# Optimization experiments

Hardware: AMD Instinct MI355X
Metric: run time of the kernel (lower is better)

The kernel has to match this reference:

```python
import jax, jax.numpy as jnp
import numpy as np

# Model dims (see init_kwargs)
NU = 4096   # num_users (one-hot feature dim)
NV = 4096   # num_items
C = 5       # num_classes (rating levels)
H0 = 256    # hidden[0]
H1 = 128    # hidden[1]
D_IN = 512  # input_dim (side-feature dense dim)
SIDE = 1024 # raw side-feature dim (u_features.size(1))
NB = 2      # nb basis matrices in bilinear decoder


def setup_inputs() -> dict:
    key = jax.random.key(0)
    ks = jax.random.split(key, 16)
    u = jax.random.randint(ks[0], (4096,), 0, NU)
    v = jax.random.randint(ks[1], (4096,), 0, NV)
    r = jax.random.randint(ks[2], (4096,), 0, C)  # unused by forward (as in source)
    raw = jax.random.randint(ks[3], (NU, NV), 0, 4 * C)
    adj_matrix = (raw[None, :, :] == jnp.arange(1, C + 1)[:, None, None]).astype(jnp.float32)
    u_features = jax.random.normal(ks[4], (NU, SIDE), jnp.float32)
    v_features = jax.random.normal(ks[5], (NV, SIDE), jnp.float32)
    def w(k, shape, fan):
        return jax.random.normal(k, shape, jnp.float32) / np.float32(np.sqrt(fan))
    u_w = w(ks[6], (C, NU, H0), NU)          # per-relation GraphConvolution user weights
    v_w = w(ks[7], (C, NV, H0), NV)          # per-relation item weights
    Wu1 = w(ks[8], (D_IN, SIDE), SIDE); bu1 = jnp.zeros((D_IN,), jnp.float32)
    Wv1 = w(ks[9], (D_IN, SIDE), SIDE); bv1 = jnp.zeros((D_IN,), jnp.float32)
    Wu2 = w(ks[10], (H1, D_IN + H0), D_IN + H0)
    Wv2 = w(ks[11], (H1, D_IN + H0), D_IN + H0)
    P = w(ks[12], (NB, H1, H1), H1)          # bilinear basis matrices
    a = w(ks[13], (NB, C), NB)               # basis -> class coefficients
    return dict(u=u, v=v, r=r, adj_matrix=adj_matrix, u_features=u_features,
                v_features=v_features, u_w=u_w, v_w=v_w, Wu1=Wu1, bu1=bu1,
                Wv1=Wv1, bv1=bv1, Wu2=Wu2, Wv2=Wv2, P=P, a=a)


def reference(u, v, r, adj_matrix, u_features, v_features, u_w, v_w,
              Wu1, bu1, Wv1, bv1, Wu2, Wv2, P, a):
    # m = adj[:, u][:, :, v]  -> [C, nu, nv]
    m = adj_matrix[:, u][:, :, v]
    # degree normalization exactly as written in gc_encoder
    du = jnp.abs(m.sum(axis=1).sum(axis=0))   # [nv]
    di = jnp.abs(m.sum(axis=2).sum(axis=0))   # [nu]
    c = 1.0 / jnp.concatenate([du, di], axis=0)
    c = jnp.where(jnp.isinf(c), jnp.zeros_like(c), c)
    # ordinal weight sharing: W_r = sum_{s<=r} Theta_s; one-hot feat @ W == gather rows
    cu = jnp.cumsum(u_w, axis=0)              # [C, NU, H0]
    cv = jnp.cumsum(v_w, axis=0)
    u_x = cu[:, u]                            # [C, nu, H0]
    v_x = cv[:, v]                            # [C, nv, H0]
    # accumulate per-relation message passing across all C relations at once
    u_next = jnp.einsum('ruv,rvh->uh', m, v_x)   # [nu, H0]
    v_next = jnp.einsum('ruv,ruh->vh', m, u_x)   # [nv, H0]
    z = jax.nn.relu(jnp.concatenate([u_next, v_next], axis=0) * c[:, None])
    nu = u.shape[0]
    u_z, v_z = z[:nu], z[nu:]
    u_f = jax.nn.relu(u_features[u] @ Wu1.T + bu1)
    v_f = jax.nn.relu(v_features[v] @ Wv1.T + bv1)
    u_h = jax.nn.relu(jnp.concatenate([u_z, u_f], axis=1) @ Wu2.T)   # [nu, H1]
    v_h = jax.nn.relu(jnp.concatenate([v_z, v_f], axis=1) @ Wv2.T)   # [nv, H1]
    # bilinear mixture decoder: logits[c,u,v] = sum_b a[b,c] * u_h Q_b v_h^T
    outputs = jnp.einsum('ud,bde,ve,bc->cuv', u_h, P, v_h, a)        # [C, nu, nv]
    logp = jax.nn.log_softmax(outputs, axis=0)
    prob = jnp.exp(logp)
    ratings = jnp.arange(1, C + 1, dtype=outputs.dtype)
    m_hat = jnp.einsum('c,cuv->uv', ratings, prob)
    # losses over observed entries
    mask = m.sum(axis=0) > 0
    n_obs = jnp.maximum(mask.sum(), 1).astype(outputs.dtype)
    loss = -(m * logp).sum() / n_obs
    target = (jnp.argmax(m, axis=0) + 1).astype(outputs.dtype)
    se = jnp.where(mask, (m_hat - target) ** 2, jnp.zeros_like(m_hat))
    rmse_loss = jnp.sqrt(se.sum() / n_obs)
    return (m_hat, loss, rmse_loss)
```

## Files before the change

kernel.cpp:

```cpp
#include <hip/hip_runtime.h>
#include <stdint.h>

#define N4   4096
#define H0   256
#define SIDE 1024
#define DIN  512
#define HCAT 768
#define H1   128
#define NC   5
#define NUV  16777216ULL
#define CAP  1536

typedef __attribute__((ext_vector_type(8))) short short8;
typedef __attribute__((ext_vector_type(4))) float floatx4;

__device__ __forceinline__ unsigned short f2bf(float f) {
    unsigned int u;
    __builtin_memcpy(&u, &f, 4);
    unsigned int r = (u + 0x7FFFu + ((u >> 16) & 1u)) >> 16;
    return (unsigned short)r;
}

__device__ __forceinline__ float bf2f(unsigned short b) {
    unsigned int u = (unsigned int)b << 16;
    float f;
    __builtin_memcpy(&f, &u, 4);
    return f;
}

__global__ __launch_bounds__(256) void k_codeF(const float* __restrict__ adj,
                                               uchar4* __restrict__ code4,
                                               const int* __restrict__ u,
                                               const int* __restrict__ v,
                                               int* __restrict__ cu,
                                               int* __restrict__ cv) {
    int b = blockIdx.x, t = threadIdx.x;
    if (b < 16384) {
        size_t g = (size_t)b * 256 + t;
        size_t base = g * 4;
        uchar4 out = {0, 0, 0, 0};
        #pragma unroll
        for (int c = 0; c < NC; c++) {
            float4 s = *(const float4*)(adj + (size_t)c * NUV + base);
            out.x = (s.x != 0.f) ? (unsigned char)(c + 1) : out.x;
            out.y = (s.y != 0.f) ? (unsigned char)(c + 1) : out.y;
            out.z = (s.z != 0.f) ? (unsigned char)(c + 1) : out.z;
            out.w = (s.w != 0.f) ? (unsigned char)(c + 1) : out.w;
        }
        code4[g] = out;
    } else {
        int i = (b - 16384) * 256 + t;
        atomicAdd(&cu[u[i]], 1);
        atomicAdd(&cv[v[i]], 1);
    }
}

__global__ __launch_bounds__(256) void k_fuse0(const uint8_t* __restrict__ code,
                                               uint8_t* __restrict__ codeT,
                                               const float* __restrict__ u_w,
                                               const int* __restrict__ cnt_u,
                                               unsigned short* __restrict__ T_Au,
                                               const float* __restrict__ v_w,
                                               const int* __restrict__ cnt_v,
                                               unsigned short* __restrict__ T_Bv) {
    __shared__ __align__(16) uint8_t tile[64][80];
    int b = blockIdx.x, t = threadIdx.x;
    if (b < 4096) {
        int bx = b & 63, by = b >> 6;
        int row = t >> 2;
        int seg = (t & 3) * 16;
        int p0 = by * 64, q0 = bx * 64;
        uint4 vdat = *(const uint4*)(code + (size_t)(p0 + row) * N4 + q0 + seg);
        *(uint4*)(&tile[row][seg]) = vdat;
        __syncthreads();
        union { uint4 u4; uint8_t bb[16]; } o;
        #pragma unroll
        for (int l = 0; l < 16; l++) o.bb[l] = tile[seg + l][row];
        *(uint4*)(codeT + (size_t)(q0 + row) * N4 + p0 + seg) = o.u4;
    } else {
        int node = (b - 4096) & 4095;
        int side = (b - 4096) >> 12;
        const float* w = side ? v_w : u_w;
        const int* cnt = side ? cnt_v : cnt_u;
        unsigned short* out = side ? T_Bv : T_Au;
        int h = t;
        float c = (float)cnt[node];
        float acc = 0.f;
        #pragma unroll
        for (int r = 0; r < NC; r++) {
            size_t idx = ((size_t)r * N4 + node) * H0 + h;
            acc += w[idx];
            union { _Float16 h16; unsigned short s; } cvt;
            cvt.h16 = (_Float16)(acc * c);
            out[idx] = cvt.s;
        }
    }
}

__global__ __launch_bounds__(256) void k_compactF(const uint8_t* __restrict__ code,
                                                  const uint8_t* __restrict__ codeT,
                                                  const int* __restrict__ cnt_u,
                                                  const int* __restrict__ cnt_v,
                                                  unsigned short* __restrict__ idxU,
                                                  int* __restrict__ nnzU,
                                                  float* __restrict__ rowDeg,
                                                  unsigned short* __restrict__ idxV,
                                                  int* __restrict__ nnzV,
                                                  float* __restrict__ colDeg) {
    __shared__ float cw[4096];
    __shared__ int wtot[4];
    __shared__ float wdeg[4];
    __shared__ unsigned short ebuf[CAP];
    int side = blockIdx.y;
    const uint8_t* codeRows = side ? codeT : code;
    const int* cntOther = side ? cnt_u : cnt_v;
    unsigned short* idx = side ? idxV : idxU;
    int* nnz = side ? nnzV : nnzU;
    float* deg = side ? colDeg : rowDeg;

    int p = blockIdx.x, t = threadIdx.x;
    int lane = t & 63, wv = t >> 6;
    const int4* co4 = (const int4*)cntOther;
    #pragma unroll
    for (int l = 0; l < 4; l++) {
        int4 ci = co4[t + l * 256];
        ((float4*)cw)[t + l * 256] =
            make_float4((float)ci.x, (float)ci.y, (float)ci.z, (float)ci.w);
    }
    uint4 w = ((const uint4*)(codeRows + (size_t)p * N4))[t];
    unsigned char b[16];
    __builtin_memcpy(b, &w, 16);
    int cnt = 0;
    #pragma unroll
    for (int j = 0; j < 16; j++) cnt += (b[j] != 0);
    int sc = cnt;
    #pragma unroll
    for (int off = 1; off < 64; off <<= 1) {
        int up = __shfl_up(sc, off, 64);
        if (lane >= off) sc += up;
    }
    if (lane == 63) wtot[wv] = sc;
    __syncthreads();
    int wbase = 0;
    #pragma unroll
    for (int ww = 0; ww < 4; ww++) wbase += (ww < wv) ? wtot[ww] : 0;
    int total = wtot[0] + wtot[1] + wtot[2] + wtot[3];
    int pos = wbase + sc - cnt;
    float dsum = 0.f;
    #pragma unroll
    for (int j = 0; j < 16; j++) {
        int r = b[j];
        if (r) {
            int q = t * 16 + j;
            if (pos < CAP) ebuf[pos] = (unsigned short)((r - 1) * N4 + q);
            pos++;
            dsum += cw[q];
        }
    }
    #pragma unroll
    for (int off = 32; off; off >>= 1) dsum += __shfl_down(dsum, off, 64);
    if (lane == 0) wdeg[wv] = dsum;
    __syncthreads();
    int tw = total < CAP ? total : CAP;
    if (t == 0) { deg[p] = wdeg[0] + wdeg[1] + wdeg[2] + wdeg[3]; nnz[p] = tw; }
    for (int e = t; e < tw; e += 256) idx[(size_t)p * CAP + e] = ebuf[e];
}

__global__ __launch_bounds__(256) void k_gatherF(const unsigned short* __restrict__ idxU,
                                                 const int* __restrict__ nnzU,
                                                 const unsigned short* __restrict__ T_Bv,
                                                 float* __restrict__ u_nn,
                                                 const unsigned short* __restrict__ idxV,
                                                 const int* __restrict__ nnzV,
                                                 const unsigned short* __restrict__ T_Au,
                                                 float* __restrict__ v_nn) {
    __shared__ unsigned short sidx[CAP];
    __shared__ float red[16][132];
    int side = blockIdx.z;
    const unsigned short* idx = side ? idxV : idxU;
    const int* nnz = side ? nnzV : nnzU;
    const char* tb = (const char*)(side ? T_Au : T_Bv);
    float* outNN = side ? v_nn : u_nn;

    int p = blockIdx.x, half = blockIdx.y, t = threadIdx.x;
    int n = nnz[p];
    const unsigned short* rowIdx = idx + (size_t)p * CAP;
    for (int i = t; i < n; i += 256) sidx[i] = rowIdx[i];
    __syncthreads();
    int s = t >> 4;
    int c = t & 15;
    int boff = half * 256 + c * 16;
    float acc[8] = {0.f, 0.f, 0.f, 0.f, 0.f, 0.f, 0.f, 0.f};
    int nmain = n & ~63;
    for (int e = s; e < nmain; e += 64) {
        int o0 = ((int)sidx[e])      << 9;
        int o1 = ((int)sidx[e + 16]) << 9;
        int o2 = ((int)sidx[e + 32]) << 9;
        int o3 = ((int)sidx[e + 48]) << 9;
        uint4 d0 = *(const uint4*)(tb + o0 + boff);
        uint4 d1 = *(const uint4*)(tb + o1 + boff);
        uint4 d2 = *(const uint4*)(tb + o2 + boff);
        uint4 d3 = *(const uint4*)(tb + o3 + boff);
        union { uint4 u; _Float16 h[8]; } cv;
        cv.u = d0;
        #pragma unroll
        for (int k = 0; k < 8; k++) acc[k] += (float)cv.h[k];
        cv.u = d1;
        #pragma unroll
        for (int k = 0; k < 8; k++) acc[k] += (float)cv.h[k];
        cv.u = d2;
        #pragma unroll
        for (int k = 0; k < 8; k++) acc[k] += (float)cv.h[k];
        cv.u = d3;
        #pragma unroll
        for (int k = 0; k < 8; k++) acc[k] += (float)cv.h[k];
    }
    for (int e = nmain + s; e < n; e += 16) {
        int o = ((int)sidx[e]) << 9;
        uint4 d = *(const uint4*)(tb + o + boff);
        union { uint4 u; _Float16 h[8]; } cv;
        cv.u = d;
        #pragma unroll
        for (int k = 0; k < 8; k++) acc[k] += (float)cv.h[k];
    }
    #pragma unroll
    for (int k = 0; k < 8; k++) red[s][c * 8 + k] = acc[k];
    __syncthreads();
    if (t < 128) {
        float sum = 0.f;
        #pragma unroll
        for (int ss = 0; ss < 16; ss++) sum += red[ss][t];
        outNN[(size_t)p * H0 + half * 128 + t] = sum;
    }
}

__global__ __launch_bounds__(256) void k_fuse1(const uint8_t* __restrict__ code,
                                               const int* __restrict__ u,
                                               const int* __restrict__ v,
                                               uint8_t* __restrict__ codeR,
                                               const float* __restrict__ u_nn,
                                               const float* __restrict__ v_nn,
                                               const float* __restrict__ colDeg,
                                               const float* __restrict__ rowDeg,
                                               unsigned short* __restrict__ chiU,
                                               unsigned short* __restrict__ cloU,
                                               unsigned short* __restrict__ chiV,
                                               unsigned short* __restrict__ cloV,
                                               const float* __restrict__ u_feat,
                                               unsigned short* __restrict__ fuhi,
                                               unsigned short* __restrict__ fulo,
                                               const float* __restrict__ v_feat,
                                               unsigned short* __restrict__ fvhi,
                                               unsigned short* __restrict__ fvlo,
                                               const float* __restrict__ Wu1,
                                               unsigned short* __restrict__ wuhi,
                                               unsigned short* __restrict__ wulo,
                                               const float* __restrict__ Wv1,
                                               unsigned short* __restrict__ wvhi,
                                               unsigned short* __restrict__ wvlo,
                                               const float* __restrict__ Wu2,
                                               unsigned short* __restrict__ w2uhi,
                                               unsigned short* __restrict__ w2ulo,
                                               const float* __restrict__ Wv2,
                                               unsigned short* __restrict__ w2vhi,
                                               unsigned short* __restrict__ w2vlo,
                                               const float* __restrict__ P,
                                               float* __restrict__ Pt) {
    __shared__ __align__(16) uint8_t rowbuf[4096];
    int b = blockIdx.x, t = threadIdx.x;
    if (b < 4096) {
        int i = b;
        int urow = u[i];
        ((uint4*)rowbuf)[t] = ((const uint4*)(code + (size_t)urow * N4))[t];
        __syncthreads();
        uint8_t ob[16];
        #pragma unroll
        for (int w = 0; w < 4; w++) {
            int4 vv = ((const int4*)v)[t * 4 + w];
            ob[w * 4 + 0] = rowbuf[vv.x];
            ob[w * 4 + 1] = rowbuf[vv.y];
            ob[w * 4 + 2] = rowbuf[vv.z];
            ob[w * 4 + 3] = rowbuf[vv.w];
        }
        uint4 o;
        __builtin_memcpy(&o, ob, 16);
        ((uint4*)(codeR + (size_t)i * N4))[t] = o;
        return;
    }
    if (b < 12288) {
        int i = (b - 4096) & 4095;
        int side = (b - 4096) >> 12;
        const float* nn = side ? v_nn : u_nn;
        const int* idxs = side ? v : u;
        const int* idxo = side ? u : v;
        const float* deg = side ? rowDeg : colDeg;
        unsigned short* catHi = side ? chiV : chiU;
        unsigned short* catLo = side ? cloV : cloU;
        int h = t;
        float d = deg[idxo[i]];
        float inv = d > 0.f ? 1.f / d : 0.f;
        float val = fmaxf(nn[(size_t)idxs[i] * H0 + h] * inv, 0.f);
        unsigned short hb = f2bf(val);
        catHi[(size_t)i * HCAT + h] = hb;
        catLo[(size_t)i * HCAT + h] = f2bf(val - bf2f(hb));
        return;
    }
    if (b >= 21696) {
        int tid = (b - 21696) * 256 + t;
        int bb = tid >> 14;
        int d = (tid >> 7) & 127;
        int e = tid & 127;
        Pt[((size_t)bb * 128 + e) * 128 + d] = P[tid];
        return;
    }
    const float* src;
    unsigned short* hi;
    unsigned short* lo;
    int lb;
    if (b < 16384)      { src = u_feat; hi = fuhi; lo = fulo; lb = b - 12288; }
    else if (b < 20480) { src = v_feat; hi = fvhi; lo = fvlo; lb = b - 16384; }
    else if (b < 20992) { src = Wu1; hi = wuhi; lo = wulo; lb = b - 20480; }
    else if (b < 21504) { src = Wv1; hi = wvhi; lo = wvlo; lb = b - 20992; }
    else if (b < 21600) { src = Wu2; hi = w2uhi; lo = w2ulo; lb = b - 21504; }
    else                { src = Wv2; hi = w2vhi; lo = w2vlo; lb = b - 21600; }
    size_t g = ((size_t)lb * 256 + t) * 4;
    float4 x = *(const float4*)(src + g);
    float f[4] = {x.x, x.y, x.z, x.w};
    unsigned short hh[4], ll[4];
    #pragma unroll
    for (int k = 0; k < 4; k++) {
        unsigned short hb = f2bf(f[k]);
        hh[k] = hb;
        ll[k] = f2bf(f[k] - bf2f(hb));
    }
    *(ushort4*)(hi + g) = make_ushort4(hh[0], hh[1], hh[2], hh[3]);
    *(ushort4*)(lo + g) = make_ushort4(ll[0], ll[1], ll[2], ll[3]);
}

__global__ __launch_bounds__(256) void k_l1F(const unsigned short* __restrict__ fuhi,
                                             const unsigned short* __restrict__ fulo,
                                             const unsigned short* __restrict__ fvhi,
                                             const unsigned short* __restrict__ fvlo,
                                             const int* __restrict__ u,
                                             const int* __restrict__ v,
                                             const unsigned short* __restrict__ wuhi,
                                             const unsigned short* __restrict__ wulo,
                                             const unsigned short* __restrict__ wvhi,
                                             const unsigned short* __restrict__ wvlo,
                                             const float* __restrict__ bu1,
                                             const float* __restrict__ bv1,
                                             unsigned short* __restrict__ chiU,
                                             unsigned short* __restrict__ cloU,
                                             unsigned short* __restrict__ chiV,
                                             unsigned short* __restrict__ cloV) {
    __shared__ unsigned short Bh[64][72];
    __shared__ unsigned short Bl[64][72];
    int side = blockIdx.z;
    const unsigned short* Ahi = side ? fvhi : fuhi;
    const unsigned short* Alo = side ? fvlo : fulo;
    const int* rowmap = side ? v : u;
    const unsigned short* Bhi = side ? wvhi : wuhi;
    const unsigned short* Blo = side ? wvlo : wulo;
    const float* bias = side ? bv1 : bu1;
    unsigned short* CHi = (side ? chiV : chiU) + H0;
    unsigned short* CLo = (side ? cloV : cloU) + H0;

    int t = threadIdx.x;
    int wave = t >> 6, lane = t & 63;
    int lr = lane & 15;
    int lk = lane >> 4;
    int i0 = blockIdx.y * 64 + wave * 16;
    int n0 = blockIdx.x * 64;
    int gi = rowmap[i0 + lr];
    const unsigned short* pah = Ahi + (size_t)gi * SIDE;
    const unsigned short* pal = Alo + (size_t)gi * SIDE;
    int srow = t >> 2, sseg = (t & 3) * 16;
    floatx4 acc[4];
    #pragma unroll
    for (int jt = 0; jt < 4; jt++) acc[jt] = (floatx4){0.f, 0.f, 0.f, 0.f};
    for (int ks = 0; ks < SIDE / 64; ks++) {
        const unsigned short* sh = Bhi + (size_t)(n0 + srow) * SIDE + ks * 64 + sseg;
        const unsigned short* sl = Blo + (size_t)(n0 + srow) * SIDE + ks * 64 + sseg;
        __syncthreads();
        *(uint4*)(&Bh[srow][sseg]) = *(const uint4*)sh;
        *(uint4*)(&Bh[srow][sseg + 8]) = *(const uint4*)(sh + 8);
        *(uint4*)(&Bl[srow][sseg]) = *(const uint4*)sl;
        *(uint4*)(&Bl[srow][sseg + 8]) = *(const uint4*)(sl + 8);
        __syncthreads();
        #pragma unroll
        for (int kk = 0; kk < 2; kk++) {
            int ko = ks * 64 + kk * 32 + lk * 8;
            short8 ah = *(const short8*)(pah + ko);
            short8 al = *(const short8*)(pal + ko);
            #pragma unroll
            for (int jt = 0; jt < 4; jt++) {
                short8 bh = *(const short8*)(&Bh[jt * 16 + lr][kk * 32 + lk * 8]);
                short8 bl = *(const short8*)(&Bl[jt * 16 + lr][kk * 32 + lk * 8]);
                acc[jt] = __builtin_amdgcn_mfma_f32_16x16x32_bf16(ah, bh, acc[jt], 0, 0, 0);
                acc[jt] = __builtin_amdgcn_mfma_f32_16x16x32_bf16(ah, bl, acc[jt], 0, 0, 0);
                acc[jt] = __builtin_amdgcn_mfma_f32_16x16x32_bf16(al, bh, acc[jt], 0, 0, 0);
            }
        }
    }
    #pragma unroll
    for (int jt = 0; jt < 4; jt++) {
        int cn = n0 + jt * 16 + lr;
        float bb = bias[cn];
        #pragma unroll
        for (int r = 0; r < 4; r++) {
            int ci = i0 + lk * 4 + r;
            float vv = fmaxf(acc[jt][r] + bb, 0.f);
            unsigned short hb = f2bf(vv);
            CHi[(size_t)ci * HCAT + cn] = hb;
            CLo[(size_t)ci * HCAT + cn] = f2bf(vv - bf2f(hb));
        }
    }
}

__global__ __launch_bounds__(256) void k_l2F(const unsigned short* __restrict__ chiU,
                                             const unsigned short* __restrict__ cloU,
                                             const unsigned short* __restrict__ w2uhi,
                                             const unsigned short* __restrict__ w2ulo,
                                             float* __restrict__ uh,
                                             const unsigned short* __restrict__ chiV,
                                             const unsigned short* __restrict__ cloV,
                                             const unsigned short* __restrict__ w2vhi,
                                             const unsigned short* __restrict__ w2vlo,
                                             unsigned short* __restrict__ vhb) {
    __shared__ unsigned short Bh[64][72];
    __shared__ unsigned short Bl[64][72];
    int side = blockIdx.z;
    const unsigned short* Ahi = side ? chiV : chiU;
    const unsigned short* Alo = side ? cloV : cloU;
    const unsigned short* Bhi = side ? w2vhi : w2uhi;
    const unsigned short* Blo = side ? w2vlo : w2ulo;

    int t = threadIdx.x;
    int wave = t >> 6, lane = t & 63;
    int lr = lane & 15;
    int lk = lane >> 4;
    int i0 = blockIdx.y * 64 + wave * 16;
    int n0 = blockIdx.x * 64;
    const unsigned short* pah = Ahi + (size_t)(i0 + lr) * HCAT;
    const unsigned short* pal = Alo + (size_t)(i0 + lr) * HCAT;
    int srow = t >> 2, sseg = (t & 3) * 16;
    floatx4 acc[4];
    #pragma unroll
    for (int jt = 0; jt < 4; jt++) acc[jt] = (floatx4){0.f, 0.f, 0.f, 0.f};
    for (int ks = 0; ks < HCAT / 64; ks++) {
        const unsigned short* sh = Bhi + (size_t)(n0 + srow) * HCAT + ks * 64 + sseg;
        const unsigned short* sl = Blo + (size_t)(n0 + srow) * HCAT + ks * 64 + sseg;
        __syncthreads();
        *(uint4*)(&Bh[srow][sseg]) = *(const uint4*)sh;
        *(uint4*)(&Bh[srow][sseg + 8]) = *(const uint4*)(sh + 8);
        *(uint4*)(&Bl[srow][sseg]) = *(const uint4*)sl;
        *(uint4*)(&Bl[srow][sseg + 8]) = *(const uint4*)(sl + 8);
        __syncthreads();
        #pragma unroll
        for (int kk = 0; kk < 2; kk++) {
            int ko = ks * 64 + kk * 32 + lk * 8;
            short8 ah = *(const short8*)(pah + ko);
            short8 al = *(const short8*)(pal + ko);
            #pragma unroll
            for (int jt = 0; jt < 4; jt++) {
                short8 bh = *(const short8*)(&Bh[jt * 16 + lr][kk * 32 + lk * 8]);
                short8 bl = *(const short8*)(&Bl[jt * 16 + lr][kk * 32 + lk * 8]);
                acc[jt] = __builtin_amdgcn_mfma_f32_16x16x32_bf16(ah, bh, acc[jt], 0, 0, 0);
                acc[jt] = __builtin_amdgcn_mfma_f32_16x16x32_bf16(ah, bl, acc[jt], 0, 0, 0);
                acc[jt] = __builtin_amdgcn_mfma_f32_16x16x32_bf16(al, bh, acc[jt], 0, 0, 0);
            }
        }
    }
    #pragma unroll
    for (int jt = 0; jt < 4; jt++) {
        int cn = n0 + jt * 16 + lr;
        #pragma unroll
        for (int r = 0; r < 4; r++) {
            int ci = i0 + lk * 4 + r;
            float vv = fmaxf(acc[jt][r], 0.f);
            if (side) {
                vhb[(size_t)ci * H1 + cn] = f2bf(vv);
            } else {
                uh[(size_t)ci * H1 + cn] = vv;
            }
        }
    }
}

template <int TM, int TN, int BK, int RM, int RN>
__global__ __launch_bounds__(256) void k_gemm(const float* __restrict__ A, int lda,
                                              const float* __restrict__ B, int ldb,
                                              float* __restrict__ C, int ldc, int K,
                                              size_t bzs, size_t czs) {
    constexpr int TX = TN / RN;
    constexpr int TY = TM / RM;
    static_assert(TX * TY == 256, "block must be 256");
    __shared__ float As[BK][TM + 4];
    __shared__ float Bs[BK][TN + 4];
    int tid = threadIdx.x;
    int tx = tid % TX, ty = tid / TX;
    int i0 = blockIdx.x * TM, n0 = blockIdx.y * TN;
    const float* Bz = B + (size_t)blockIdx.z * bzs;
    float acc[RM][RN] = {};
    for (int k0 = 0; k0 < K; k0 += BK) {
        for (int g = tid; g < TM * BK / 4; g += 256) {
            int i = g / (BK / 4), kc = g % (BK / 4);
            float4 val = *(const float4*)(A + (size_t)(i0 + i) * lda + k0 + kc * 4);
            As[kc * 4 + 0][i] = val.x; As[kc * 4 + 1][i] = val.y;
            As[kc * 4 + 2][i] = val.z; As[kc * 4 + 3][i] = val.w;
        }
        for (int g = tid; g < TN * BK / 4; g += 256) {
            int n = g / (BK / 4), kc = g % (BK / 4);
            float4 val = *(const float4*)(Bz + (size_t)(n0 + n) * ldb + k0 + kc * 4);
            Bs[kc * 4 + 0][n] = val.x; Bs[kc * 4 + 1][n] = val.y;
            Bs[kc * 4 + 2][n] = val.z; Bs[kc * 4 + 3][n] = val.w;
        }
        __syncthreads();
        #pragma unroll
        for (int k = 0; k < BK; k++) {
            float av[RM], bv[RN];
            #pragma unroll
            for (int m = 0; m < RM; m++) av[m] = As[k][ty * RM + m];
            #pragma unroll
            for (int n = 0; n < RN; n++) bv[n] = Bs[k][tx * RN + n];
            #pragma unroll
            for (int m = 0; m < RM; m++)
                #pragma unroll
                for (int n = 0; n < RN; n++)
                    acc[m][n] = fmaf(av[m], bv[n], acc[m][n]);
        }
        __syncthreads();
    }
    #pragma unroll
    for (int m = 0; m < RM; m++) {
        int ig = i0 + ty * RM + m;
        #pragma unroll
        for (int n = 0; n < RN; n++) {
            unsigned short* Cz16 = (unsigned short*)C + (size_t)blockIdx.z * czs;
            Cz16[(size_t)ig * ldc + n0 + tx * RN + n] = f2bf(acc[m][n]);
        }
    }
}

__global__ __launch_bounds__(256) void k_scores3(const unsigned short* __restrict__ tb,
                                                 const unsigned short* __restrict__ vhb,
                                                 const uint8_t* __restrict__ codeR,
                                                 const float* __restrict__ a_f,
                                                 float* __restrict__ mhat,
                                                 float* __restrict__ part) {
    __shared__ float wred[4][3];
    int t = threadIdx.x;
    int wave = t >> 6, lane = t & 63;
    int lr = lane & 15;
    int lk = lane >> 4;
    int i0 = blockIdx.y * 64 + wave * 16;
    int j0 = blockIdx.x * 128;
    float sa0[NC], sa1[NC];
    #pragma unroll
    for (int c = 0; c < NC; c++) { sa0[c] = a_f[c]; sa1[c] = a_f[5 + c]; }

    const unsigned short* t0p = tb;
    const unsigned short* t1p = tb + (size_t)N4 * H1;
    short8 a0[4], a1[4];
    #pragma unroll
    for (int kc = 0; kc < 4; kc++) {
        size_t off = (size_t)(i0 + lr) * H1 + kc * 32 + lk * 8;
        a0[kc] = *(const short8*)(t0p + off);
        a1[kc] = *(const short8*)(t1p + off);
    }

    const uint8_t* crbase = codeR + (size_t)(i0 + lk * 4) * N4 + lr;
    short8 bcur[4];
    int cbv[4];
    {
        int jb = j0;
        const uint8_t* crp = crbase + jb;
        cbv[0] = crp[0];
        cbv[1] = crp[N4];
        cbv[2] = crp[2 * N4];
        cbv[3] = crp[3 * N4];
        #pragma unroll
        for (int kc = 0; kc < 4; kc++)
            bcur[kc] = *(const short8*)(vhb + (size_t)(jb + lr) * H1 + kc * 32 + lk * 8);
    }

    float lsum = 0.f, ssum = 0.f, nobs = 0.f;
    for (int jt = 0; jt < 8; jt++) {
        int jb = j0 + jt * 16;
        int j = jb + lr;
        short8 bnext[4];
        int cbn[4];
        if (jt < 7) {
            int jb2 = jb + 16;
            const uint8_t* crp = crbase + jb2;
            cbn[0] = crp[0];
            cbn[1] = crp[N4];
            cbn[2] = crp[2 * N4];
            cbn[3] = crp[3 * N4];
            #pragma unroll
            for (int kc = 0; kc < 4; kc++)
                bnext[kc] = *(const short8*)(vhb + (size_t)(jb2 + lr) * H1 + kc * 32 + lk * 8);
        }
        floatx4 C0 = {0.f, 0.f, 0.f, 0.f}, C1 = {0.f, 0.f, 0.f, 0.f};
        #pragma unroll
        for (int kc = 0; kc < 4; kc++) {
            C0 = __builtin_amdgcn_mfma_f32_16x16x32_bf16(a0[kc], bcur[kc], C0, 0, 0, 0);
            C1 = __builtin_amdgcn_mfma_f32_16x16x32_bf16(a1[kc], bcur[kc], C1, 0, 0, 0);
        }
        #pragma unroll
        for (int r = 0; r < 4; r++) {
            int i = i0 + lk * 4 + r;
            float v0 = C0[r], v1 = C1[r];
            float l[NC];
            float mx = -1e30f;
            #pragma unroll
            for (int c = 0; c < NC; c++) {
                l[c] = sa0[c] * v0 + sa1[c] * v1;
                mx = fmaxf(mx, l[c]);
            }
            float den = 0.f, num = 0.f;
            #pragma unroll
            for (int c = 0; c < NC; c++) {
                float e = __expf(l[c] - mx);
                den += e;
                num += (float)(c + 1) * e;
            }
            float mh = num / den;
            mhat[(size_t)i * N4 + j] = mh;
            int cb = cbv[r];
            if (cb) {
                float lse = mx + __logf(den);
                lsum += lse - l[cb - 1];
                float df = mh - (float)cb;
                ssum += df * df;
                nobs += 1.f;
            }
        }
        if (jt < 7) {
            #pragma unroll
            for (int kc = 0; kc < 4; kc++) bcur[kc] = bnext[kc];
            #pragma unroll
            for (int r = 0; r < 4; r++) cbv[r] = cbn[r];
        }
    }
    #pragma unroll
    for (int off = 32; off; off >>= 1) {
        lsum += __shfl_down(lsum, off, 64);
        ssum += __shfl_down(ssum, off, 64);
        nobs += __shfl_down(nobs, off, 64);
    }
    if (lane == 0) { wred[wave][0] = lsum; wred[wave][1] = ssum; wred[wave][2] = nobs; }
    __syncthreads();
    if (t == 0) {
        int bid = blockIdx.y * gridDim.x + blockIdx.x;
        part[bid * 3 + 0] = wred[0][0] + wred[1][0] + wred[2][0] + wred[3][0];
        part[bid * 3 + 1] = wred[0][1] + wred[1][1] + wred[2][1] + wred[3][1];
        part[bid * 3 + 2] = wred[0][2] + wred[1][2] + wred[2][2] + wred[3][2];
    }
}

__global__ __launch_bounds__(256) void k_finalize(const float* __restrict__ part,
                                                  float* __restrict__ out) {
    __shared__ float sred[3][4];
    int t = threadIdx.x, lane = t & 63, wv = t >> 6;
    float l = 0.f, s = 0.f, n = 0.f;
    for (int i = t; i < 2048; i += 256) {
        l += part[i * 3 + 0];
        s += part[i * 3 + 1];
        n += part[i * 3 + 2];
    }
    #pragma unroll
    for (int off = 32; off; off >>= 1) {
        l += __shfl_down(l, off, 64);
        s += __shfl_down(s, off, 64);
        n += __shfl_down(n, off, 64);
    }
    if (lane == 0) { sred[0][wv] = l; sred[1][wv] = s; sred[2][wv] = n; }
    __syncthreads();
    if (t == 0) {
        float L = sred[0][0] + sred[0][1] + sred[0][2] + sred[0][3];
        float S = sred[1][0] + sred[1][1] + sred[1][2] + sred[1][3];
        float N = fmaxf(sred[2][0] + sred[2][1] + sred[2][2] + sred[2][3], 1.f);
        out[NUV + 0] = L / N;
        out[NUV + 1] = sqrtf(S / N);
    }
}

extern "C" void kernel_launch(void* const* d_in, const int* in_sizes, int n_in,
                              void* d_out, int out_size, void* d_ws, size_t ws_size,
                              hipStream_t stream) {
    const int* u = (const int*)d_in[0];
    const int* v = (const int*)d_in[1];
    const float* adj    = (const float*)d_in[3];
    const float* u_feat = (const float*)d_in[4];
    const float* v_feat = (const float*)d_in[5];
    const float* u_w    = (const float*)d_in[6];
    const float* v_w    = (const float*)d_in[7];
    const float* Wu1    = (const float*)d_in[8];
    const float* bu1    = (const float*)d_in[9];
    const float* Wv1    = (const float*)d_in[10];
    const float* bv1    = (const float*)d_in[11];
    const float* Wu2    = (const float*)d_in[12];
    const float* Wv2    = (const float*)d_in[13];
    const float* P      = (const float*)d_in[14];
    const float* a      = (const float*)d_in[15];
    float* out = (float*)d_out;

    char* ws = (char*)d_ws;
    const size_t O_CODE  = 0;
    const size_t O_CNTU  = 16777216;
    const size_t O_CNTV  = O_CNTU + 16384;
    const size_t O_ACC   = O_CNTV + 16384;
    const size_t O_TAU   = O_ACC + 256;
    const size_t O_TBV   = O_TAU + 10485760;
    const size_t O_IDXU  = O_TBV + 10485760;
    const size_t O_IDXV  = O_IDXU + 12582912;
    const size_t O_NNZU  = O_IDXV + 12582912;
    const size_t O_NNZV  = O_NNZU + 16384;
    const size_t O_RDEG  = O_NNZV + 16384;
    const size_t O_CDEG  = O_RDEG + 16384;
    const size_t O_UNN   = O_CDEG + 16384;
    const size_t O_VNN   = O_UNN + 4194304;
    const size_t O_UCAT  = O_VNN + 4194304;
    const size_t O_VCAT  = O_UCAT + 12582912;
    const size_t O_UH    = O_VCAT + 12582912;
    const size_t O_VHB   = O_UH + 2097152;
    const size_t O_PT    = O_VHB + 1048576;
    const size_t O_TB    = O_PT + 131072;
    const size_t O_CODET = O_UCAT;
    const size_t O_CODER = O_TAU;
    const size_t O_PART  = O_CNTU;
    const size_t O_FUHI  = O_IDXU;
    const size_t O_FULO  = O_IDXV;
    const size_t O_CHIU  = O_UCAT;
    const size_t O_CLOU  = O_UCAT + 6291456;
    const size_t O_CHIV  = O_VCAT;
    const size_t O_CLOV  = O_VCAT + 6291456;
    const size_t S_FVHI  = 0;
    const size_t S_FVLO  = 8388608;
    const size_t S_WUHI  = 16777216;
    const size_t S_WULO  = S_WUHI + 1048576;
    const size_t S_WVHI  = S_WULO + 1048576;
    const size_t S_WVLO  = S_WVHI + 1048576;
    const size_t S_W2UHI = S_WVLO + 1048576;
    const size_t S_W2ULO = S_W2UHI + 196608;
    const size_t S_W2VHI = S_W2ULO + 196608;
    const size_t S_W2VLO = S_W2VHI + 196608;

    uint8_t* code  = (uint8_t*)(ws + O_CODE);
    uint8_t* codeT = (uint8_t*)(ws + O_CODET);
    uint8_t* codeR = (uint8_t*)(ws + O_CODER);
    int* cnt_u = (int*)(ws + O_CNTU);
    int* cnt_v = (int*)(ws + O_CNTV);
    unsigned short* T_Au = (unsigned short*)(ws + O_TAU);
    unsigned short* T_Bv = (unsigned short*)(ws + O_TBV);
    unsigned short* idxU = (unsigned short*)(ws + O_IDXU);
    unsigned short* idxV = (unsigned short*)(ws + O_IDXV);
    int* nnzU = (int*)(ws + O_NNZU);
    int* nnzV = (int*)(ws + O_NNZV);
    float* rowDeg = (float*)(ws + O_RDEG);
    float* colDeg = (float*)(ws + O_CDEG);
    float* u_nn = (float*)(ws + O_UNN);
    float* v_nn = (float*)(ws + O_VNN);
    float* uh = (float*)(ws + O_UH);
    unsigned short* vhb = (unsigned short*)(ws + O_VHB);
    float* Pt = (float*)(ws + O_PT);
    unsigned short* tb = (unsigned short*)(ws + O_TB);
    float* part = (float*)(ws + O_PART);
    unsigned short* fuhi = (unsigned short*)(ws + O_FUHI);
    unsigned short* fulo = (unsigned short*)(ws + O_FULO);
    unsigned short* chiU = (unsigned short*)(ws + O_CHIU);
    unsigned short* cloU = (unsigned short*)(ws + O_CLOU);
    unsigned short* chiV = (unsigned short*)(ws + O_CHIV);
    unsigned short* cloV = (unsigned short*)(ws + O_CLOV);
    char* outc = (char*)d_out;
    unsigned short* fvhi = (unsigned short*)(outc + S_FVHI);
    unsigned short* fvlo = (unsigned short*)(outc + S_FVLO);
    unsigned short* wuhi = (unsigned short*)(outc + S_WUHI);
    unsigned short* wulo = (unsigned short*)(outc + S_WULO);
    unsigned short* wvhi = (unsigned short*)(outc + S_WVHI);
    unsigned short* wvlo = (unsigned short*)(outc + S_WVLO);
    unsigned short* w2uhi = (unsigned short*)(outc + S_W2UHI);
    unsigned short* w2ulo = (unsigned short*)(outc + S_W2ULO);
    unsigned short* w2vhi = (unsigned short*)(outc + S_W2VHI);
    unsigned short* w2vlo = (unsigned short*)(outc + S_W2VLO);

    hipMemsetAsync(ws + O_CNTU, 0, 16384 + 16384, stream);

    k_codeF<<<16400, 256, 0, stream>>>(adj, (uchar4*)code, u, v, cnt_u, cnt_v);
    k_fuse0<<<12288, 256, 0, stream>>>(code, codeT, u_w, cnt_u, T_Au, v_w, cnt_v, T_Bv);
    k_compactF<<<dim3(N4, 2), 256, 0, stream>>>(code, codeT, cnt_u, cnt_v,
                                                idxU, nnzU, rowDeg, idxV, nnzV, colDeg);
    k_gatherF<<<dim3(N4, 2, 2), 256, 0, stream>>>(idxU, nnzU, T_Bv, u_nn,
                                                  idxV, nnzV, T_Au, v_nn);
    k_fuse1<<<21824, 256, 0, stream>>>(code, u, v, codeR, u_nn, v_nn, colDeg, rowDeg,
                                       chiU, cloU, chiV, cloV,
                                       u_feat, fuhi, fulo,
                                       v_feat, fvhi, fvlo,
                                       Wu1, wuhi, wulo, Wv1, wvhi, wvlo,
                                       Wu2, w2uhi, w2ulo, Wv2, w2vhi, w2vlo,
                                       P, Pt);
    k_l1F<<<dim3(8, 64, 2), 256, 0, stream>>>(fuhi, fulo, fvhi, fvlo, u, v,
                                              wuhi, wulo, wvhi, wvlo, bu1, bv1,
                                              chiU, cloU, chiV, cloV);
    k_l2F<<<dim3(2, 64, 2), 256, 0, stream>>>(chiU, cloU, w2uhi, w2ulo, uh,
                                              chiV, cloV, w2vhi, w2vlo, vhb);
    k_gemm<64, 32, 16, 4, 2>
        <<<dim3(64, 4, 2), 256, 0, stream>>>(uh, H1, Pt, H1,
                                             (float*)tb, H1, H1,
                                             (size_t)H1 * H1, (size_t)N4 * H1);
    k_scores3<<<dim3(32, 64), 256, 0, stream>>>(tb, vhb, codeR, a, out, part);
    k_finalize<<<1, 256, 0, stream>>>(part, out);
}
```

Measured before the change: 891.8 us.

## Split sparse gather into column-range epochs with partial sums reduced in fuse1

The gather kernel now splits each row's nonzero list into four column-range epochs, found by binary search over the sorted indices. Blocks are ordered epoch-major so the gathered table rows touched at any moment fit a smaller window, which is meant to improve L2/MALL locality. Each epoch writes a partial sum to a scratch buffer placed in the output region, and k_fuse1 adds the four partials. Index loads into shared memory are vectorized to 16 bytes. The cost is four times more blocks, each re-loading the row's index list and running a binary search, plus extra partial-sum traffic.

```diff
diff --git a/kernel.cpp b/kernel.cpp
--- a/kernel.cpp
+++ b/kernel.cpp
@@ -110,7 +110,7 @@
     __shared__ float cw[4096];
     __shared__ int wtot[4];
     __shared__ float wdeg[4];
-    __shared__ unsigned short ebuf[CAP];
+    __shared__ __align__(16) unsigned short ebuf[CAP];
     int side = blockIdx.y;
     const uint8_t* codeRows = side ? codeT : code;
     const int* cntOther = side ? cnt_u : cnt_v;
@@ -166,33 +166,55 @@
     for (int e = t; e < tw; e += 256) idx[(size_t)p * CAP + e] = ebuf[e];
 }
 
-__global__ __launch_bounds__(256) void k_gatherF(const unsigned short* __restrict__ idxU,
+__global__ __launch_bounds__(256) void k_gatherE(const unsigned short* __restrict__ idxU,
                                                  const int* __restrict__ nnzU,
                                                  const unsigned short* __restrict__ T_Bv,
-                                                 float* __restrict__ u_nn,
                                                  const unsigned short* __restrict__ idxV,
                                                  const int* __restrict__ nnzV,
                                                  const unsigned short* __restrict__ T_Au,
-                                                 float* __restrict__ v_nn) {
-    __shared__ unsigned short sidx[CAP];
+                                                 float* __restrict__ pnn) {
+    __shared__ __align__(16) unsigned short sidx[CAP];
     __shared__ float red[16][132];
-    int side = blockIdx.z;
+    __shared__ int sbnd[2];
+    int bid = blockIdx.x;
+    int side  = bid >> 15;
+    int r1    = bid & 32767;
+    int epoch = r1 >> 13;
+    int r2    = r1 & 8191;
+    int p     = r2 >> 1;
+    int half  = r2 & 1;
+
     const unsigned short* idx = side ? idxV : idxU;
     const int* nnz = side ? nnzV : nnzU;
     const char* tb = (const char*)(side ? T_Au : T_Bv);
-    float* outNN = side ? v_nn : u_nn;
-
-    int p = blockIdx.x, half = blockIdx.y, t = threadIdx.x;
+
+    int t = threadIdx.x;
     int n = nnz[p];
     const unsigned short* rowIdx = idx + (size_t)p * CAP;
-    for (int i = t; i < n; i += 256) sidx[i] = rowIdx[i];
+    int nv = (n + 7) >> 3;
+    for (int i = t; i < nv; i += 256)
+        ((uint4*)sidx)[i] = ((const uint4*)rowIdx)[i];
     __syncthreads();
+    if (t < 2) {
+        int target = (epoch + t) << 10;
+        int lo = 0, hi = n;
+        while (lo < hi) {
+            int mid = (lo + hi) >> 1;
+            int q = sidx[mid] & 4095;
+            if (q < target) lo = mid + 1; else hi = mid;
+        }
+        sbnd[t] = lo;
+    }
+    __syncthreads();
+    int elo = sbnd[0], ehi = sbnd[1];
+
     int s = t >> 4;
     int c = t & 15;
     int boff = half * 256 + c * 16;
     float acc[8] = {0.f, 0.f, 0.f, 0.f, 0.f, 0.f, 0.f, 0.f};
-    int nmain = n & ~63;
-    for (int e = s; e < nmain; e += 64) {
+    int cnt = ehi - elo;
+    int nmain = elo + (cnt & ~63);
+    for (int e = elo + s; e < nmain; e += 64) {
         int o0 = ((int)sidx[e])      << 9;
         int o1 = ((int)sidx[e + 16]) << 9;
         int o2 = ((int)sidx[e + 32]) << 9;
@@ -215,7 +237,7 @@
         #pragma unroll
         for (int k = 0; k < 8; k++) acc[k] += (float)cv.h[k];
     }
-    for (int e = nmain + s; e < n; e += 16) {
+    for (int e = nmain + s; e < ehi; e += 16) {
         int o = ((int)sidx[e]) << 9;
         uint4 d = *(const uint4*)(tb + o + boff);
         union { uint4 u; _Float16 h[8]; } cv;
@@ -230,7 +252,7 @@
         float sum = 0.f;
         #pragma unroll
         for (int ss = 0; ss < 16; ss++) sum += red[ss][t];
-        outNN[(size_t)p * H0 + half * 128 + t] = sum;
+        pnn[(((size_t)(side * 4 + epoch)) * N4 + p) * H0 + half * 128 + t] = sum;
     }
 }
 
@@ -238,8 +260,7 @@
                                                const int* __restrict__ u,
                                                const int* __restrict__ v,
                                                uint8_t* __restrict__ codeR,
-                                               const float* __restrict__ u_nn,
-                                               const float* __restrict__ v_nn,
+                                               const float* __restrict__ pnn,
                                                const float* __restrict__ colDeg,
                                                const float* __restrict__ rowDeg,
                                                unsigned short* __restrict__ chiU,
@@ -290,7 +311,6 @@
     if (b < 12288) {
         int i = (b - 4096) & 4095;
         int side = (b - 4096) >> 12;
-        const float* nn = side ? v_nn : u_nn;
         const int* idxs = side ? v : u;
         const int* idxo = side ? u : v;
         const float* deg = side ? rowDeg : colDeg;
@@ -299,7 +319,12 @@
         int h = t;
         float d = deg[idxo[i]];
         float inv = d > 0.f ? 1.f / d : 0.f;
-        float val = fmaxf(nn[(size_t)idxs[i] * H0 + h] * inv, 0.f);
+        int row = idxs[i];
+        const float* pr = pnn + ((size_t)side * 4 * N4 + row) * H0 + h;
+        float nnv = 0.f;
+        #pragma unroll
+        for (int e = 0; e < 4; e++) nnv += pr[(size_t)e * N4 * H0];
+        float val = fmaxf(nnv * inv, 0.f);
         unsigned short hb = f2bf(val);
         catHi[(size_t)i * HCAT + h] = hb;
         catLo[(size_t)i * HCAT + h] = f2bf(val - bf2f(hb));
@@ -353,8 +378,8 @@
                                              unsigned short* __restrict__ cloU,
                                              unsigned short* __restrict__ chiV,
                                              unsigned short* __restrict__ cloV) {
-    __shared__ unsigned short Bh[64][72];
-    __shared__ unsigned short Bl[64][72];
+    __shared__ __align__(16) unsigned short Bh[64][72];
+    __shared__ __align__(16) unsigned short Bl[64][72];
     int side = blockIdx.z;
     const unsigned short* Ahi = side ? fvhi : fuhi;
     const unsigned short* Alo = side ? fvlo : fulo;
@@ -427,8 +452,8 @@
                                              const unsigned short* __restrict__ w2vhi,
                                              const unsigned short* __restrict__ w2vlo,
                                              unsigned short* __restrict__ vhb) {
-    __shared__ unsigned short Bh[64][72];
-    __shared__ unsigned short Bl[64][72];
+    __shared__ __align__(16) unsigned short Bh[64][72];
+    __shared__ __align__(16) unsigned short Bl[64][72];
     int side = blockIdx.z;
     const unsigned short* Ahi = side ? chiV : chiU;
     const unsigned short* Alo = side ? cloV : cloU;
@@ -746,6 +771,7 @@
     const size_t S_W2ULO = S_W2UHI + 196608;
     const size_t S_W2VHI = S_W2ULO + 196608;
     const size_t S_W2VLO = S_W2VHI + 196608;
+    const size_t S_PNN   = 25165824;
 
     uint8_t* code  = (uint8_t*)(ws + O_CODE);
     uint8_t* codeT = (uint8_t*)(ws + O_CODET);
@@ -760,8 +786,6 @@
     int* nnzV = (int*)(ws + O_NNZV);
     float* rowDeg = (float*)(ws + O_RDEG);
     float* colDeg = (float*)(ws + O_CDEG);
-    float* u_nn = (float*)(ws + O_UNN);
-    float* v_nn = (float*)(ws + O_VNN);
     float* uh = (float*)(ws + O_UH);
     unsigned short* vhb = (unsigned short*)(ws + O_VHB);
     float* Pt = (float*)(ws + O_PT);
@@ -784,6 +808,7 @@
     unsigned short* w2ulo = (unsigned short*)(outc + S_W2ULO);
     unsigned short* w2vhi = (unsigned short*)(outc + S_W2VHI);
     unsigned short* w2vlo = (unsigned short*)(outc + S_W2VLO);
+    float* pnn = (float*)(outc + S_PNN);
 
     hipMemsetAsync(ws + O_CNTU, 0, 16384 + 16384, stream);
 
@@ -791,9 +816,8 @@
     k_fuse0<<<12288, 256, 0, stream>>>(code, codeT, u_w, cnt_u, T_Au, v_w, cnt_v, T_Bv);
     k_compactF<<<dim3(N4, 2), 256, 0, stream>>>(code, codeT, cnt_u, cnt_v,
                                                 idxU, nnzU, rowDeg, idxV, nnzV, colDeg);
-    k_gatherF<<<dim3(N4, 2, 2), 256, 0, stream>>>(idxU, nnzU, T_Bv, u_nn,
-                                                  idxV, nnzV, T_Au, v_nn);
-    k_fuse1<<<21824, 256, 0, stream>>>(code, u, v, codeR, u_nn, v_nn, colDeg, rowDeg,
+    k_gatherE<<<65536, 256, 0, stream>>>(idxU, nnzU, T_Bv, idxV, nnzV, T_Au, pnn);
+    k_fuse1<<<21824, 256, 0, stream>>>(code, u, v, codeR, pnn, colDeg, rowDeg,
                                        chiU, cloU, chiV, cloV,
                                        u_feat, fuhi, fulo,
                                        v_feat, fvhi, fvlo,
```

Measured after the change: 881.8 us. No clear change (-1.1%).
